# Optimization experiments

Measured on AMD Instinct MI355X. Metric: run time of the kernel, lower is better.

Reference implementation:

```python
import jax, jax.numpy as jnp
import numpy as np

B, HOP, D = 32768, 32, 64  # batch, hop_number (neighbor samples), embed dim (ent == rel)


def setup_inputs() -> dict:
    key = jax.random.key(0)
    ks = jax.random.split(key, 7)
    s = 0.1  # mimic glorot-scale init for weights
    return {
        "entity": jax.random.normal(ks[0], (B, 1, D), dtype=jnp.float32),
        "relation": jax.random.normal(ks[1], (B, HOP, D), dtype=jnp.float32),
        "neighbor": jax.random.normal(ks[2], (B, HOP, D), dtype=jnp.float32),
        "w_h": jax.random.normal(ks[3], (D, D), dtype=jnp.float32) * s,
        "w_t": jax.random.normal(ks[4], (D, D), dtype=jnp.float32) * s,
        "w_r": jax.random.normal(ks[5], (D, D), dtype=jnp.float32) * s,
        "v_a": jax.random.normal(ks[6], (3 * D, 1), dtype=jnp.float32) * s,
    }


def reference(entity, relation, neighbor, w_h, w_t, w_r, v_a):
    # entity: (B,1,D); relation/neighbor: (B,HOP,D)
    b, hop, _ = relation.shape
    # f_entity = zeros_like(relation[:,:,0]).reshape(-1, hop, 1)  -> all zeros
    f_entity = jnp.zeros((b, hop, 1), dtype=relation.dtype)
    # K.batch_dot(f_entity, entity, [2,1]): (B,HOP,1)x(B,1,D) -> (B,HOP,D) (zeros)
    entity_hat = jnp.einsum('bhi,bid->bhd', f_entity, entity)
    head_entity = entity_hat @ w_h            # (B,HOP,D)
    rel = relation @ w_r                      # (B,HOP,D)
    tail_entity = neighbor @ w_t              # (B,HOP,D)
    head_rel_tail = jnp.concatenate([head_entity, rel, tail_entity], axis=-1)  # (B,HOP,3D)
    scores = jnp.tanh(head_rel_tail) @ v_a    # (B,HOP,1)
    return jax.nn.softmax(scores, axis=-2)    # softmax over hop axis
```

## Files before the change

kernel.cpp:

```cpp
#include <hip/hip_runtime.h>


typedef short bf16x8 __attribute__((ext_vector_type(8)));
typedef float f32x4 __attribute__((ext_vector_type(4)));

#define NB   32768
#define NHOP 32
#define ND   64

__device__ __forceinline__ float tanh_fast(float x) {
  float cx = fminf(fmaxf(x, -20.f), 20.f);
  float e2 = __expf(2.f * cx);
  return (e2 - 1.f) * __builtin_amdgcn_rcpf(e2 + 1.f);
}

__device__ __forceinline__ void split2(float4 v0, float4 v1, bf16x8 &hi, bf16x8 &lo) {
  float xs[8] = {v0.x, v0.y, v0.z, v0.w, v1.x, v1.y, v1.z, v1.w};
#pragma unroll
  for (int j = 0; j < 8; ++j) {
    unsigned u = __builtin_bit_cast(unsigned, xs[j]);
    hi[j] = (short)(u >> 16);
    float hif = __builtin_bit_cast(float, u & 0xffff0000u);
    lo[j] = (short)(__builtin_bit_cast(unsigned, xs[j] - hif) >> 16);
  }
}

__global__ __launch_bounds__(256, 2)
void attn_fused(const float* __restrict__ rel, const float* __restrict__ nbr,
                const float* __restrict__ wr, const float* __restrict__ wt,
                const float* __restrict__ va, float* __restrict__ out, int nwaves) {
  const int lane = threadIdx.x & 63;
  const int wid  = (blockIdx.x * blockDim.x + threadIdx.x) >> 6;
  const int l15  = lane & 15;
  const int lg   = lane >> 4;

  bf16x8 wf[2][2][4][2];
#pragma unroll
  for (int mat = 0; mat < 2; ++mat) {
    const float* W = mat ? wt : wr;
#pragma unroll
    for (int c = 0; c < 2; ++c)
#pragma unroll
      for (int nt = 0; nt < 4; ++nt) {
        bf16x8 hi, lo;
#pragma unroll
        for (int j = 0; j < 8; ++j) {
          float x = W[(c * 32 + lg * 8 + j) * 64 + nt * 16 + l15];
          unsigned u = __builtin_bit_cast(unsigned, x);
          hi[j] = (short)(u >> 16);
          float hif = __builtin_bit_cast(float, u & 0xffff0000u);
          lo[j] = (short)(__builtin_bit_cast(unsigned, x - hif) >> 16);
        }
        wf[mat][c][nt][0] = hi;
        wf[mat][c][nt][1] = lo;
      }
  }

  float va1[4], va2[4];
#pragma unroll
  for (int nt = 0; nt < 4; ++nt) {
    va1[nt] = va[64 + nt * 16 + l15];
    va2[nt] = va[128 + nt * 16 + l15];
  }

  for (int b = wid; b < NB; b += nwaves) {
    float sc[2][4];
#pragma unroll
    for (int tt = 0; tt < 2; ++tt) {
      const size_t row = (size_t)b * NHOP + tt * 16 + l15;
      const float* rbase = rel + row * ND + lg * 8;
      const float* tbase = nbr + row * ND + lg * 8;
      float4 r0 = *(const float4*)(rbase);
      float4 r1 = *(const float4*)(rbase + 4);
      float4 r2 = *(const float4*)(rbase + 32);
      float4 r3 = *(const float4*)(rbase + 36);
      float4 t0 = *(const float4*)(tbase);
      float4 t1 = *(const float4*)(tbase + 4);
      float4 t2 = *(const float4*)(tbase + 32);
      float4 t3 = *(const float4*)(tbase + 36);

      f32x4 part = {0.f, 0.f, 0.f, 0.f};

      {
        bf16x8 ahi[2], alo[2];
        split2(r0, r1, ahi[0], alo[0]);
        split2(r2, r3, ahi[1], alo[1]);
        f32x4 acc[4];
#pragma unroll
        for (int nt = 0; nt < 4; ++nt) acc[nt] = (f32x4){0.f, 0.f, 0.f, 0.f};
#pragma unroll
        for (int c = 0; c < 2; ++c)
#pragma unroll
          for (int nt = 0; nt < 4; ++nt) {
            acc[nt] = __builtin_amdgcn_mfma_f32_16x16x32_bf16(ahi[c], wf[0][c][nt][0], acc[nt], 0, 0, 0);
            acc[nt] = __builtin_amdgcn_mfma_f32_16x16x32_bf16(alo[c], wf[0][c][nt][0], acc[nt], 0, 0, 0);
            acc[nt] = __builtin_amdgcn_mfma_f32_16x16x32_bf16(ahi[c], wf[0][c][nt][1], acc[nt], 0, 0, 0);
          }
#pragma unroll
        for (int nt = 0; nt < 4; ++nt)
#pragma unroll
          for (int rr = 0; rr < 4; ++rr)
            part[rr] += tanh_fast(acc[nt][rr]) * va1[nt];
      }

      {
        bf16x8 ahi[2], alo[2];
        split2(t0, t1, ahi[0], alo[0]);
        split2(t2, t3, ahi[1], alo[1]);
        f32x4 acc[4];
#pragma unroll
        for (int nt = 0; nt < 4; ++nt) acc[nt] = (f32x4){0.f, 0.f, 0.f, 0.f};
#pragma unroll
        for (int c = 0; c < 2; ++c)
#pragma unroll
          for (int nt = 0; nt < 4; ++nt) {
            acc[nt] = __builtin_amdgcn_mfma_f32_16x16x32_bf16(ahi[c], wf[1][c][nt][0], acc[nt], 0, 0, 0);
            acc[nt] = __builtin_amdgcn_mfma_f32_16x16x32_bf16(alo[c], wf[1][c][nt][0], acc[nt], 0, 0, 0);
            acc[nt] = __builtin_amdgcn_mfma_f32_16x16x32_bf16(ahi[c], wf[1][c][nt][1], acc[nt], 0, 0, 0);
          }
#pragma unroll
        for (int nt = 0; nt < 4; ++nt)
#pragma unroll
          for (int rr = 0; rr < 4; ++rr)
            part[rr] += tanh_fast(acc[nt][rr]) * va2[nt];
      }

#pragma unroll
      for (int m = 1; m <= 8; m <<= 1)
#pragma unroll
        for (int rr = 0; rr < 4; ++rr)
          part[rr] += __shfl_xor(part[rr], m, 64);
#pragma unroll
      for (int rr = 0; rr < 4; ++rr) sc[tt][rr] = part[rr];
    }

    float smax = fmaxf(fmaxf(sc[0][0], sc[0][1]), fmaxf(sc[0][2], sc[0][3]));
    smax = fmaxf(smax, fmaxf(fmaxf(sc[1][0], sc[1][1]), fmaxf(sc[1][2], sc[1][3])));
    smax = fmaxf(smax, __shfl_xor(smax, 16, 64));
    smax = fmaxf(smax, __shfl_xor(smax, 32, 64));

    float e[2][4];
    float ssum = 0.f;
#pragma unroll
    for (int tt = 0; tt < 2; ++tt)
#pragma unroll
      for (int rr = 0; rr < 4; ++rr) {
        e[tt][rr] = __expf(sc[tt][rr] - smax);
        ssum += e[tt][rr];
      }
    ssum += __shfl_xor(ssum, 16, 64);
    ssum += __shfl_xor(ssum, 32, 64);
    float inv = __builtin_amdgcn_rcpf(ssum);

    if (l15 == 0) {
      float* ob = out + (size_t)b * NHOP;
      float4 o0 = {e[0][0] * inv, e[0][1] * inv, e[0][2] * inv, e[0][3] * inv};
      float4 o1 = {e[1][0] * inv, e[1][1] * inv, e[1][2] * inv, e[1][3] * inv};
      *(float4*)(ob + lg * 4)      = o0;
      *(float4*)(ob + 16 + lg * 4) = o1;
    }
  }
}

extern "C" void kernel_launch(void* const* d_in, const int* in_sizes, int n_in,
                              void* d_out, int out_size, void* d_ws, size_t ws_size,
                              hipStream_t stream) {
  const float* rel = (const float*)d_in[1];
  const float* nbr = (const float*)d_in[2];
  const float* wt  = (const float*)d_in[4];
  const float* wr  = (const float*)d_in[5];
  const float* va  = (const float*)d_in[6];
  float* out = (float*)d_out;

  const int blocks = 1024;
  attn_fused<<<blocks, 256, 0, stream>>>(rel, nbr, wr, wt, va, out, blocks * 4);
}
```

Measured before the change: 532.1 us.

## Stage split weights in LDS, hoist all loads, use DPP reductions, raise occupancy

The hi/lo bf16 weight fragments move from per-thread registers into shared memory, filled cooperatively by the four waves of a block. This frees VGPRs so launch bounds go from 2 to 3 blocks per CU, and the grid doubles. The loop now issues all relation and neighbor loads for a batch element up front and interleaves the two hop tiles in the MFMA chain. The per-row cross-lane sums use DPP row operations instead of xor shuffles. The cost is LDS reads of the weight fragments on every iteration and one block barrier at start.

```diff
diff --git a/kernel.cpp b/kernel.cpp
--- a/kernel.cpp
+++ b/kernel.cpp
@@ -25,114 +25,117 @@
   }
 }
 
-__global__ __launch_bounds__(256, 2)
+__device__ __forceinline__ float dpp_reduce16(float x) {
+  int t;
+  t = __builtin_amdgcn_update_dpp(0, __builtin_bit_cast(int, x), 0xB1, 0xf, 0xf, true);
+  x += __builtin_bit_cast(float, t);
+  t = __builtin_amdgcn_update_dpp(0, __builtin_bit_cast(int, x), 0x4E, 0xf, 0xf, true);
+  x += __builtin_bit_cast(float, t);
+  t = __builtin_amdgcn_update_dpp(0, __builtin_bit_cast(int, x), 0x141, 0xf, 0xf, true);
+  x += __builtin_bit_cast(float, t);
+  t = __builtin_amdgcn_update_dpp(0, __builtin_bit_cast(int, x), 0x140, 0xf, 0xf, true);
+  x += __builtin_bit_cast(float, t);
+  return x;
+}
+
+__global__ __launch_bounds__(256, 3)
 void attn_fused(const float* __restrict__ rel, const float* __restrict__ nbr,
                 const float* __restrict__ wr, const float* __restrict__ wt,
                 const float* __restrict__ va, float* __restrict__ out, int nwaves) {
+  __shared__ bf16x8 wlds[32][64];
+
   const int lane = threadIdx.x & 63;
+  const int wv   = threadIdx.x >> 6;
   const int wid  = (blockIdx.x * blockDim.x + threadIdx.x) >> 6;
   const int l15  = lane & 15;
   const int lg   = lane >> 4;
 
-  bf16x8 wf[2][2][4][2];
 #pragma unroll
-  for (int mat = 0; mat < 2; ++mat) {
+  for (int i = 0; i < 4; ++i) {
+    int combo = wv * 4 + i;
+    int mat = combo >> 3, c = (combo >> 2) & 1, nt = combo & 3;
     const float* W = mat ? wt : wr;
+    bf16x8 hi, lo;
 #pragma unroll
-    for (int c = 0; c < 2; ++c)
-#pragma unroll
-      for (int nt = 0; nt < 4; ++nt) {
-        bf16x8 hi, lo;
-#pragma unroll
-        for (int j = 0; j < 8; ++j) {
-          float x = W[(c * 32 + lg * 8 + j) * 64 + nt * 16 + l15];
-          unsigned u = __builtin_bit_cast(unsigned, x);
-          hi[j] = (short)(u >> 16);
-          float hif = __builtin_bit_cast(float, u & 0xffff0000u);
-          lo[j] = (short)(__builtin_bit_cast(unsigned, x - hif) >> 16);
-        }
-        wf[mat][c][nt][0] = hi;
-        wf[mat][c][nt][1] = lo;
-      }
+    for (int j = 0; j < 8; ++j) {
+      float x = W[(c * 32 + lg * 8 + j) * 64 + nt * 16 + l15];
+      unsigned u = __builtin_bit_cast(unsigned, x);
+      hi[j] = (short)(u >> 16);
+      float hif = __builtin_bit_cast(float, u & 0xffff0000u);
+      lo[j] = (short)(__builtin_bit_cast(unsigned, x - hif) >> 16);
+    }
+    wlds[combo * 2][lane]     = hi;
+    wlds[combo * 2 + 1][lane] = lo;
   }
+  __syncthreads();
 
-  float va1[4], va2[4];
+  float vaa[2][4];
 #pragma unroll
   for (int nt = 0; nt < 4; ++nt) {
-    va1[nt] = va[64 + nt * 16 + l15];
-    va2[nt] = va[128 + nt * 16 + l15];
+    vaa[0][nt] = va[64 + nt * 16 + l15];
+    vaa[1][nt] = va[128 + nt * 16 + l15];
   }
 
   for (int b = wid; b < NB; b += nwaves) {
-    float sc[2][4];
+    float4 raw[2][2][4];
 #pragma unroll
-    for (int tt = 0; tt < 2; ++tt) {
-      const size_t row = (size_t)b * NHOP + tt * 16 + l15;
-      const float* rbase = rel + row * ND + lg * 8;
-      const float* tbase = nbr + row * ND + lg * 8;
-      float4 r0 = *(const float4*)(rbase);
-      float4 r1 = *(const float4*)(rbase + 4);
-      float4 r2 = *(const float4*)(rbase + 32);
-      float4 r3 = *(const float4*)(rbase + 36);
-      float4 t0 = *(const float4*)(tbase);
-      float4 t1 = *(const float4*)(tbase + 4);
-      float4 t2 = *(const float4*)(tbase + 32);
-      float4 t3 = *(const float4*)(tbase + 36);
+    for (int mat = 0; mat < 2; ++mat) {
+      const float* src = mat ? nbr : rel;
+#pragma unroll
+      for (int tt = 0; tt < 2; ++tt) {
+        const float* base = src + ((size_t)b * NHOP + tt * 16 + l15) * ND + lg * 8;
+        raw[mat][tt][0] = *(const float4*)(base);
+        raw[mat][tt][1] = *(const float4*)(base + 4);
+        raw[mat][tt][2] = *(const float4*)(base + 32);
+        raw[mat][tt][3] = *(const float4*)(base + 36);
+      }
+    }
 
-      f32x4 part = {0.f, 0.f, 0.f, 0.f};
+    float sc[2][4] = {{0.f, 0.f, 0.f, 0.f}, {0.f, 0.f, 0.f, 0.f}};
 
-      {
-        bf16x8 ahi[2], alo[2];
-        split2(r0, r1, ahi[0], alo[0]);
-        split2(r2, r3, ahi[1], alo[1]);
-        f32x4 acc[4];
 #pragma unroll
-        for (int nt = 0; nt < 4; ++nt) acc[nt] = (f32x4){0.f, 0.f, 0.f, 0.f};
+    for (int mat = 0; mat < 2; ++mat) {
+      bf16x8 ahi[2][2], alo[2][2];
 #pragma unroll
-        for (int c = 0; c < 2; ++c)
+      for (int tt = 0; tt < 2; ++tt) {
+        split2(raw[mat][tt][0], raw[mat][tt][1], ahi[tt][0], alo[tt][0]);
+        split2(raw[mat][tt][2], raw[mat][tt][3], ahi[tt][1], alo[tt][1]);
+      }
+      f32x4 acc[2][4];
 #pragma unroll
-          for (int nt = 0; nt < 4; ++nt) {
-            acc[nt] = __builtin_amdgcn_mfma_f32_16x16x32_bf16(ahi[c], wf[0][c][nt][0], acc[nt], 0, 0, 0);
-            acc[nt] = __builtin_amdgcn_mfma_f32_16x16x32_bf16(alo[c], wf[0][c][nt][0], acc[nt], 0, 0, 0);
-            acc[nt] = __builtin_amdgcn_mfma_f32_16x16x32_bf16(ahi[c], wf[0][c][nt][1], acc[nt], 0, 0, 0);
+      for (int tt = 0; tt < 2; ++tt)
+#pragma unroll
+        for (int nt = 0; nt < 4; ++nt) acc[tt][nt] = (f32x4){0.f, 0.f, 0.f, 0.f};
+
+#pragma unroll
+      for (int c = 0; c < 2; ++c)
+#pragma unroll
+        for (int nt = 0; nt < 4; ++nt) {
+          int combo = (mat * 2 + c) * 4 + nt;
+          bf16x8 whi = wlds[combo * 2][lane];
+          bf16x8 wlo = wlds[combo * 2 + 1][lane];
+#pragma unroll
+          for (int tt = 0; tt < 2; ++tt) {
+            acc[tt][nt] = __builtin_amdgcn_mfma_f32_16x16x32_bf16(ahi[tt][c], whi, acc[tt][nt], 0, 0, 0);
+            acc[tt][nt] = __builtin_amdgcn_mfma_f32_16x16x32_bf16(alo[tt][c], whi, acc[tt][nt], 0, 0, 0);
+            acc[tt][nt] = __builtin_amdgcn_mfma_f32_16x16x32_bf16(ahi[tt][c], wlo, acc[tt][nt], 0, 0, 0);
           }
+        }
+
+#pragma unroll
+      for (int tt = 0; tt < 2; ++tt)
 #pragma unroll
         for (int nt = 0; nt < 4; ++nt)
 #pragma unroll
           for (int rr = 0; rr < 4; ++rr)
-            part[rr] += tanh_fast(acc[nt][rr]) * va1[nt];
-      }
-
-      {
-        bf16x8 ahi[2], alo[2];
-        split2(t0, t1, ahi[0], alo[0]);
-        split2(t2, t3, ahi[1], alo[1]);
-        f32x4 acc[4];
-#pragma unroll
-        for (int nt = 0; nt < 4; ++nt) acc[nt] = (f32x4){0.f, 0.f, 0.f, 0.f};
-#pragma unroll
-        for (int c = 0; c < 2; ++c)
-#pragma unroll
-          for (int nt = 0; nt < 4; ++nt) {
-            acc[nt] = __builtin_amdgcn_mfma_f32_16x16x32_bf16(ahi[c], wf[1][c][nt][0], acc[nt], 0, 0, 0);
-            acc[nt] = __builtin_amdgcn_mfma_f32_16x16x32_bf16(alo[c], wf[1][c][nt][0], acc[nt], 0, 0, 0);
-            acc[nt] = __builtin_amdgcn_mfma_f32_16x16x32_bf16(ahi[c], wf[1][c][nt][1], acc[nt], 0, 0, 0);
-          }
-#pragma unroll
-        for (int nt = 0; nt < 4; ++nt)
-#pragma unroll
-          for (int rr = 0; rr < 4; ++rr)
-            part[rr] += tanh_fast(acc[nt][rr]) * va2[nt];
-      }
+            sc[tt][rr] += tanh_fast(acc[tt][nt][rr]) * vaa[mat][nt];
+    }
 
 #pragma unroll
-      for (int m = 1; m <= 8; m <<= 1)
+    for (int tt = 0; tt < 2; ++tt)
 #pragma unroll
-        for (int rr = 0; rr < 4; ++rr)
-          part[rr] += __shfl_xor(part[rr], m, 64);
-#pragma unroll
-      for (int rr = 0; rr < 4; ++rr) sc[tt][rr] = part[rr];
-    }
+      for (int rr = 0; rr < 4; ++rr)
+        sc[tt][rr] = dpp_reduce16(sc[tt][rr]);
 
     float smax = fmaxf(fmaxf(sc[0][0], sc[0][1]), fmaxf(sc[0][2], sc[0][3]));
     smax = fmaxf(smax, fmaxf(fmaxf(sc[1][0], sc[1][1]), fmaxf(sc[1][2], sc[1][3])));
@@ -172,6 +175,6 @@
   const float* va  = (const float*)d_in[6];
   float* out = (float*)d_out;
 
-  const int blocks = 1024;
+  const int blocks = 2048;
   attn_fused<<<blocks, 256, 0, stream>>>(rel, nbr, wr, wt, va, out, blocks * 4);
 }
```

Result: slower. 595.2 us (+11.9%).
